# Optimization experiments

Hardware: AMD Instinct MI355X
Metric: run time of the kernel (lower is better)

## Reference

```python
import jax, jax.numpy as jnp
from jax import lax
import numpy as np

B = 32768      # batch
D = 256        # input = hidden = output dim
DEPTH = 9      # universal_depth


def setup_inputs() -> dict:
    key = jax.random.key(0)
    ks = jax.random.split(key, 16)
    s = 1.0 / np.sqrt(D)  # keep pre-activations sane
    r = lambda k, shp, sc=s: (jax.random.normal(k, shp, jnp.float32) * sc)
    return {
        "x": jax.random.normal(ks[0], (B, D), jnp.float32),
        "lin0_w": r(ks[1], (D, D)), "lin0_b": r(ks[2], (D,), 0.1),
        "lin1_w": r(ks[3], (D, D)), "lin1_b": r(ks[4], (D,), 0.1),
        "u1_w": jax.random.normal(ks[5], (DEPTH, D, D), jnp.float32),
        "u1_cw": r(ks[6], (D, D)), "u1_cb": r(ks[7], (D,), 0.1),
        "lin2_w": r(ks[8], (D, D)), "lin2_b": r(ks[9], (D,), 0.1),
        "u2_w": jax.random.normal(ks[10], (DEPTH, D, D), jnp.float32),
        "u2_cw": r(ks[11], (D, D)), "u2_cb": r(ks[12], (D,), 0.1),
        "lino_w": r(ks[13], (D, D)), "lino_b": r(ks[14], (D,), 0.1),
    }


def _universal_layer(x, uw, cw, cb):
    """UniversalNeuralLayer.forward, vectorized.

    The circulant 'gate' matrix implements, for state s of length n:
        s'[i] = cos*s[i] - sin*s[(i+1)%n] + sin*s[(i-1)%n]
    Applied 3 times per depth with angles uw[d, j, 0..2] (j = output unit).
    The result is independent of x and of the batch index.
    """
    n = x.shape[1]
    classical = x @ cw + cb                      # [B, n]
    # angle sequence per output j, in (depth, gate) order -> [3*DEPTH, n]
    angles = jnp.transpose(uw[:, :, :3], (0, 2, 1)).reshape(-1, n)
    init = jnp.full((n, n), 1.0 / np.sqrt(n), dtype=x.dtype)  # [n_j, n_state]

    def step(s, ang):
        c = jnp.cos(ang)[:, None]
        sn = jnp.sin(ang)[:, None]
        return c * s + sn * (jnp.roll(s, 1, axis=1) - jnp.roll(s, -1, axis=1)), None

    s, _ = lax.scan(step, init, angles)
    p = s[:, 0] ** 2                             # |state[0]|^2 per output j
    return jnp.tanh(classical + p[None, :])


def reference(x, lin0_w, lin0_b, lin1_w, lin1_b, u1_w, u1_cw, u1_cb,
              lin2_w, lin2_b, u2_w, u2_cw, u2_cb, lino_w, lino_b):
    h = jax.nn.relu(x @ lin0_w.T + lin0_b)
    h = jax.nn.relu(h @ lin1_w.T + lin1_b)
    h = _universal_layer(h, u1_w, u1_cw, u1_cb)
    h = jax.nn.relu(h @ lin2_w.T + lin2_b)
    h = _universal_layer(h, u2_w, u2_cw, u2_cb)
    return jax.nn.relu(h @ lino_w.T + lino_b)
```

## Files before the change

kernel.cpp:

```cpp
#include <hip/hip_runtime.h>
#include <math.h>

#define DD 256

typedef float  f32x4  __attribute__((ext_vector_type(4)));
typedef short  bf16x8 __attribute__((ext_vector_type(8)));

__device__ __forceinline__ unsigned short f2bf(float f) {
    unsigned int u = __float_as_uint(f);
    u = (u + 0x7fffu + ((u >> 16) & 1u)) >> 16;
    return (unsigned short)u;
}
__device__ __forceinline__ float bf2f(unsigned int h16) {
    return __uint_as_float(h16 << 16);
}

__global__ __launch_bounds__(256)
void universal_p_kernel(const float* __restrict__ u1_w,
                        const float* __restrict__ u2_w,
                        float* __restrict__ p_out ) {
    const int j = threadIdx.x;
    const float* uw = blockIdx.x ? u2_w : u1_w;
    float s = 0.0625f;
#pragma unroll
    for (int d = 0; d < 9; ++d)
#pragma unroll
        for (int g = 0; g < 3; ++g)
            s *= cosf(uw[d * DD * DD + j * DD + g]);
    p_out[blockIdx.x * DD + j] = s * s;
}

__global__ __launch_bounds__(256)
void prep_weights(const float* __restrict__ w0, const float* __restrict__ w1,
                  const float* __restrict__ cw1, const float* __restrict__ w2,
                  const float* __restrict__ cw2, const float* __restrict__ wo,
                  unsigned short* __restrict__ wall) {
    const int mat = blockIdx.y;
    const int n = blockIdx.x;
    const int k = threadIdx.x;
    const float* src;
    bool tr = false;
    switch (mat) {
        case 0: src = w0; break;
        case 1: src = w1; break;
        case 2: src = cw1; tr = true; break;
        case 3: src = w2; break;
        case 4: src = cw2; tr = true; break;
        default: src = wo; break;
    }
    const float v = tr ? src[k * DD + n] : src[n * DD + k];
    wall[mat * 65536 + n * DD + k] = f2bf(v);
}

__device__ __forceinline__ int chunk_idx(int m, int kc) {
    return kc * 64 + (m ^ (kc & 7));
}

__device__ __forceinline__ float fast_tanh(float x) {
    const float e = __expf(2.0f * x);
    return 1.0f - 2.0f * __builtin_amdgcn_rcpf(1.0f + e);
}

template <int MODE>
__device__ __forceinline__ void layer_step(const uint4* hc, uint4* hn,
                                           const unsigned short* __restrict__ W,
                                           const float* __restrict__ bias,
                                           const float* __restrict__ pv) {
    const int tid  = threadIdx.x;
    const int wave = tid >> 6;
    const int lane = tid & 63;
    const int quad = lane >> 4;
    const int l15  = lane & 15;
    const int nb   = wave * 64;

    f32x4 acc[4][4];
#pragma unroll
    for (int nt = 0; nt < 4; ++nt)
#pragma unroll
        for (int mt = 0; mt < 4; ++mt) acc[nt][mt] = (f32x4){0.f, 0.f, 0.f, 0.f};

    bf16x8 w_f[2][4], h_f[2][4];
    {
        const int koff = quad * 8;
#pragma unroll
        for (int nt = 0; nt < 4; ++nt)
            w_f[0][nt] = *(const bf16x8*)&W[(nb + nt * 16 + l15) * DD + koff];
#pragma unroll
        for (int mt = 0; mt < 4; ++mt)
            h_f[0][mt] = *(const bf16x8*)&hc[chunk_idx(mt * 16 + l15, quad)];
    }
#pragma unroll
    for (int k0 = 0; k0 < 8; ++k0) {
        const int cur = k0 & 1, nxt = cur ^ 1;
        if (k0 < 7) {
            const int kc = (k0 + 1) * 4 + quad;
#pragma unroll
            for (int nt = 0; nt < 4; ++nt)
                w_f[nxt][nt] = *(const bf16x8*)&W[(nb + nt * 16 + l15) * DD + kc * 8];
#pragma unroll
            for (int mt = 0; mt < 4; ++mt)
                h_f[nxt][mt] = *(const bf16x8*)&hc[chunk_idx(mt * 16 + l15, kc)];
        }
#pragma unroll
        for (int nt = 0; nt < 4; ++nt)
#pragma unroll
            for (int mt = 0; mt < 4; ++mt)
                acc[nt][mt] = __builtin_amdgcn_mfma_f32_16x16x32_bf16(
                    w_f[cur][nt], h_f[cur][mt], acc[nt][mt], 0, 0, 0);
    }

#pragma unroll
    for (int nt = 0; nt < 4; ++nt) {
        const int n0 = nb + nt * 16 + quad * 4;
        f32x4 add = *(const f32x4*)&bias[n0];
        if (MODE == 1) add += *(const f32x4*)&pv[n0];
        const int kc_o = n0 >> 3;
        const int half = quad & 1;
#pragma unroll
        for (int mt = 0; mt < 4; ++mt) {
            const f32x4 v = acc[nt][mt] + add;
            float t0, t1, t2, t3;
            if (MODE == 1) {
                t0 = fast_tanh(v.x); t1 = fast_tanh(v.y);
                t2 = fast_tanh(v.z); t3 = fast_tanh(v.w);
            } else {
                t0 = fmaxf(v.x, 0.f); t1 = fmaxf(v.y, 0.f);
                t2 = fmaxf(v.z, 0.f); t3 = fmaxf(v.w, 0.f);
            }
            uint2 u;
            u.x = (unsigned int)f2bf(t0) | ((unsigned int)f2bf(t1) << 16);
            u.y = (unsigned int)f2bf(t2) | ((unsigned int)f2bf(t3) << 16);
            *(uint2*)((char*)&hn[chunk_idx(mt * 16 + l15, kc_o)] + half * 8) = u;
        }
    }
    __syncthreads();
}

__global__ __launch_bounds__(256, 2)
void unet_fused(const float* __restrict__ x,
                const unsigned short* __restrict__ wall,
                const float* __restrict__ b0, const float* __restrict__ b1,
                const float* __restrict__ cb1, const float* __restrict__ b2,
                const float* __restrict__ cb2, const float* __restrict__ bo,
                const float* __restrict__ pbuf,
                float* __restrict__ out) {
    __shared__ uint4 h[2][2048];
    const int m0 = blockIdx.x * 64;
    const int tid = threadIdx.x;
    const int c4 = tid & 63;
    const int rbase = (tid >> 6) * 16;
    const int kc_s = c4 >> 1;
    const int half_s = c4 & 1;

#pragma unroll
    for (int i = 0; i < 16; ++i) {
        const int row = rbase + i;
        const float4 v = *(const float4*)&x[(size_t)(m0 + row) * DD + c4 * 4];
        uint2 u;
        u.x = (unsigned int)f2bf(v.x) | ((unsigned int)f2bf(v.y) << 16);
        u.y = (unsigned int)f2bf(v.z) | ((unsigned int)f2bf(v.w) << 16);
        *(uint2*)((char*)&h[0][chunk_idx(row, kc_s)] + half_s * 8) = u;
    }
    __syncthreads();

    layer_step<0>(h[0], h[1], wall + 0 * 65536, b0, nullptr);
    layer_step<0>(h[1], h[0], wall + 1 * 65536, b1, nullptr);
    layer_step<1>(h[0], h[1], wall + 2 * 65536, cb1, pbuf);
    layer_step<0>(h[1], h[0], wall + 3 * 65536, b2, nullptr);
    layer_step<1>(h[0], h[1], wall + 4 * 65536, cb2, pbuf + 256);
    layer_step<0>(h[1], h[0], wall + 5 * 65536, bo, nullptr);

#pragma unroll
    for (int i = 0; i < 16; ++i) {
        const int row = rbase + i;
        const uint2 u = *(const uint2*)((char*)&h[0][chunk_idx(row, kc_s)] + half_s * 8);
        float4 v;
        v.x = bf2f(u.x & 0xffffu); v.y = bf2f(u.x >> 16);
        v.z = bf2f(u.y & 0xffffu); v.w = bf2f(u.y >> 16);
        *(float4*)&out[(size_t)(m0 + row) * DD + c4 * 4] = v;
    }
}

extern "C" void kernel_launch(void* const* d_in, const int* in_sizes, int n_in,
                              void* d_out, int out_size, void* d_ws, size_t ws_size,
                              hipStream_t stream) {
    const float* x      = (const float*)d_in[0];
    const float* lin0_w = (const float*)d_in[1];
    const float* lin0_b = (const float*)d_in[2];
    const float* lin1_w = (const float*)d_in[3];
    const float* lin1_b = (const float*)d_in[4];
    const float* u1_w   = (const float*)d_in[5];
    const float* u1_cw  = (const float*)d_in[6];
    const float* u1_cb  = (const float*)d_in[7];
    const float* lin2_w = (const float*)d_in[8];
    const float* lin2_b = (const float*)d_in[9];
    const float* u2_w   = (const float*)d_in[10];
    const float* u2_cw  = (const float*)d_in[11];
    const float* u2_cb  = (const float*)d_in[12];
    const float* lino_w = (const float*)d_in[13];
    const float* lino_b = (const float*)d_in[14];

    float* out = (float*)d_out;
    unsigned short* wall = (unsigned short*)d_ws;
    float* pbuf = (float*)((char*)d_ws + 6 * 65536 * 2);

    universal_p_kernel<<<dim3(2), dim3(256), 0, stream>>>(u1_w, u2_w, pbuf);
    prep_weights<<<dim3(256, 6), dim3(256), 0, stream>>>(
        lin0_w, lin1_w, u1_cw, lin2_w, u2_cw, lino_w, wall);
    unet_fused<<<dim3(512), dim3(256), 0, stream>>>(
        x, wall, lin0_b, lin1_b, u1_cb, lin2_b, u2_cb, lino_b, pbuf, out);
}
```

Baseline: 178.0 us.

## Single LDS activation buffer with 3-stage weight register prefetch across layers

```diff
diff --git a/kernel.cpp b/kernel.cpp
--- a/kernel.cpp
+++ b/kernel.cpp
@@ -61,9 +61,19 @@
     return 1.0f - 2.0f * __builtin_amdgcn_rcpf(1.0f + e);
 }
 
-template <int MODE>
-__device__ __forceinline__ void layer_step(const uint4* hc, uint4* hn,
+__device__ __forceinline__ void prefetch_W(bf16x8 (&slot)[4],
                                            const unsigned short* __restrict__ W,
+                                           int k0, int nb, int l15, int quad) {
+    const int koff = k0 * 32 + quad * 8;
+#pragma unroll
+    for (int nt = 0; nt < 4; ++nt)
+        slot[nt] = *(const bf16x8*)&W[(nb + nt * 16 + l15) * DD + koff];
+}
+
+template <int PHASE, int MODE>
+__device__ __forceinline__ void layer_step(uint4* h, bf16x8 (&wr)[3][4],
+                                           const unsigned short* __restrict__ W,
+                                           const unsigned short* __restrict__ Wn,
                                            const float* __restrict__ bias,
                                            const float* __restrict__ pv) {
     const int tid  = threadIdx.x;
@@ -79,35 +89,33 @@
 #pragma unroll
         for (int mt = 0; mt < 4; ++mt) acc[nt][mt] = (f32x4){0.f, 0.f, 0.f, 0.f};
 
-    bf16x8 w_f[2][4], h_f[2][4];
-    {
-        const int koff = quad * 8;
-#pragma unroll
-        for (int nt = 0; nt < 4; ++nt)
-            w_f[0][nt] = *(const bf16x8*)&W[(nb + nt * 16 + l15) * DD + koff];
-#pragma unroll
-        for (int mt = 0; mt < 4; ++mt)
-            h_f[0][mt] = *(const bf16x8*)&hc[chunk_idx(mt * 16 + l15, quad)];
-    }
+    bf16x8 h_f[2][4];
+#pragma unroll
+    for (int mt = 0; mt < 4; ++mt)
+        h_f[0][mt] = *(const bf16x8*)&h[chunk_idx(mt * 16 + l15, quad)];
+
 #pragma unroll
     for (int k0 = 0; k0 < 8; ++k0) {
-        const int cur = k0 & 1, nxt = cur ^ 1;
+        const int cur = (PHASE + k0) % 3;
+        const int pf  = (PHASE + k0 + 2) % 3;
+        if (k0 < 6) prefetch_W(wr[pf], W, k0 + 2, nb, l15, quad);
+        else        prefetch_W(wr[pf], Wn, k0 - 6, nb, l15, quad);
         if (k0 < 7) {
             const int kc = (k0 + 1) * 4 + quad;
 #pragma unroll
-            for (int nt = 0; nt < 4; ++nt)
-                w_f[nxt][nt] = *(const bf16x8*)&W[(nb + nt * 16 + l15) * DD + kc * 8];
-#pragma unroll
             for (int mt = 0; mt < 4; ++mt)
-                h_f[nxt][mt] = *(const bf16x8*)&hc[chunk_idx(mt * 16 + l15, kc)];
+                h_f[(k0 + 1) & 1][mt] =
+                    *(const bf16x8*)&h[chunk_idx(mt * 16 + l15, kc)];
         }
 #pragma unroll
         for (int nt = 0; nt < 4; ++nt)
 #pragma unroll
             for (int mt = 0; mt < 4; ++mt)
                 acc[nt][mt] = __builtin_amdgcn_mfma_f32_16x16x32_bf16(
-                    w_f[cur][nt], h_f[cur][mt], acc[nt][mt], 0, 0, 0);
-    }
+                    wr[cur][nt], h_f[k0 & 1][mt], acc[nt][mt], 0, 0, 0);
+    }
+
+    __syncthreads();
 
 #pragma unroll
     for (int nt = 0; nt < 4; ++nt) {
@@ -130,13 +138,13 @@
             uint2 u;
             u.x = (unsigned int)f2bf(t0) | ((unsigned int)f2bf(t1) << 16);
             u.y = (unsigned int)f2bf(t2) | ((unsigned int)f2bf(t3) << 16);
-            *(uint2*)((char*)&hn[chunk_idx(mt * 16 + l15, kc_o)] + half * 8) = u;
+            *(uint2*)((char*)&h[chunk_idx(mt * 16 + l15, kc_o)] + half * 8) = u;
         }
     }
     __syncthreads();
 }
 
-__global__ __launch_bounds__(256, 2)
+__global__ __launch_bounds__(256, 3)
 void unet_fused(const float* __restrict__ x,
                 const unsigned short* __restrict__ wall,
                 const float* __restrict__ b0, const float* __restrict__ b1,
@@ -144,14 +152,23 @@
                 const float* __restrict__ cb2, const float* __restrict__ bo,
                 const float* __restrict__ pbuf,
                 float* __restrict__ out) {
-    __shared__ uint4 h[2][2048];
+    __shared__ uint4 h[2048];
     const int m0 = blockIdx.x * 64;
     const int tid = threadIdx.x;
+    const int wave = tid >> 6;
+    const int lane = tid & 63;
+    const int quad = lane >> 4;
+    const int l15  = lane & 15;
+    const int nb   = wave * 64;
+
+    bf16x8 wr[3][4];
+    prefetch_W(wr[0], wall, 0, nb, l15, quad);
+    prefetch_W(wr[1], wall, 1, nb, l15, quad);
+
     const int c4 = tid & 63;
     const int rbase = (tid >> 6) * 16;
     const int kc_s = c4 >> 1;
     const int half_s = c4 & 1;
-
 #pragma unroll
     for (int i = 0; i < 16; ++i) {
         const int row = rbase + i;
@@ -159,21 +176,21 @@
         uint2 u;
         u.x = (unsigned int)f2bf(v.x) | ((unsigned int)f2bf(v.y) << 16);
         u.y = (unsigned int)f2bf(v.z) | ((unsigned int)f2bf(v.w) << 16);
-        *(uint2*)((char*)&h[0][chunk_idx(row, kc_s)] + half_s * 8) = u;
+        *(uint2*)((char*)&h[chunk_idx(row, kc_s)] + half_s * 8) = u;
     }
     __syncthreads();
 
-    layer_step<0>(h[0], h[1], wall + 0 * 65536, b0, nullptr);
-    layer_step<0>(h[1], h[0], wall + 1 * 65536, b1, nullptr);
-    layer_step<1>(h[0], h[1], wall + 2 * 65536, cb1, pbuf);
-    layer_step<0>(h[1], h[0], wall + 3 * 65536, b2, nullptr);
-    layer_step<1>(h[0], h[1], wall + 4 * 65536, cb2, pbuf + 256);
-    layer_step<0>(h[1], h[0], wall + 5 * 65536, bo, nullptr);
+    layer_step<0, 0>(h, wr, wall + 0 * 65536, wall + 1 * 65536, b0, nullptr);
+    layer_step<2, 0>(h, wr, wall + 1 * 65536, wall + 2 * 65536, b1, nullptr);
+    layer_step<1, 1>(h, wr, wall + 2 * 65536, wall + 3 * 65536, cb1, pbuf);
+    layer_step<0, 0>(h, wr, wall + 3 * 65536, wall + 4 * 65536, b2, nullptr);
+    layer_step<2, 1>(h, wr, wall + 4 * 65536, wall + 5 * 65536, cb2, pbuf + 256);
+    layer_step<1, 0>(h, wr, wall + 5 * 65536, wall + 0 * 65536, bo, nullptr);
 
 #pragma unroll
     for (int i = 0; i < 16; ++i) {
         const int row = rbase + i;
-        const uint2 u = *(const uint2*)((char*)&h[0][chunk_idx(row, kc_s)] + half_s * 8);
+        const uint2 u = *(const uint2*)((char*)&h[chunk_idx(row, kc_s)] + half_s * 8);
         float4 v;
         v.x = bf2f(u.x & 0xffffu); v.y = bf2f(u.x >> 16);
         v.z = bf2f(u.y & 0xffffu); v.w = bf2f(u.y >> 16);
```

Result: slower. 195.1 us (+9.6%).

## Pre-swizzle weights into MFMA fragment order and shrink row tile to 32

Applied to the files above, without the earlier changes.

```diff
diff --git a/kernel.cpp b/kernel.cpp
--- a/kernel.cpp
+++ b/kernel.cpp
@@ -35,9 +35,18 @@
                   const float* __restrict__ cw1, const float* __restrict__ w2,
                   const float* __restrict__ cw2, const float* __restrict__ wo,
                   unsigned short* __restrict__ wall) {
-    const int mat = blockIdx.y;
-    const int n = blockIdx.x;
-    const int k = threadIdx.x;
+    const int gid  = blockIdx.x * 256 + threadIdx.x;
+    const int mat  = gid >> 13;
+    const int rem  = gid & 8191;
+    const int wb   = rem >> 11;
+    const int rem2 = rem & 2047;
+    const int k0   = rem2 >> 8;
+    const int rem3 = rem2 & 255;
+    const int nt   = rem3 >> 6;
+    const int lane = rem3 & 63;
+    const int n  = wb * 64 + nt * 16 + (lane & 15);
+    const int kb = k0 * 32 + (lane >> 4) * 8;
+
     const float* src;
     bool tr = false;
     switch (mat) {
@@ -48,12 +57,18 @@
         case 4: src = cw2; tr = true; break;
         default: src = wo; break;
     }
-    const float v = tr ? src[k * DD + n] : src[n * DD + k];
-    wall[mat * 65536 + n * DD + k] = f2bf(v);
+    unsigned short tmp[8];
+#pragma unroll
+    for (int j = 0; j < 8; ++j) {
+        const float v = tr ? src[(kb + j) * DD + n] : src[n * DD + kb + j];
+        tmp[j] = f2bf(v);
+    }
+    *(uint4*)&wall[mat * 65536 + wb * 16384 + k0 * 2048 + nt * 512 + lane * 8] =
+        *(const uint4*)tmp;
 }
 
 __device__ __forceinline__ int chunk_idx(int m, int kc) {
-    return kc * 64 + (m ^ (kc & 7));
+    return kc * 32 + (m ^ (kc & 7));
 }
 
 __device__ __forceinline__ float fast_tanh(float x) {
@@ -62,8 +77,9 @@
 }
 
 template <int MODE>
-__device__ __forceinline__ void layer_step(const uint4* hc, uint4* hn,
+__device__ __forceinline__ void layer_step(uint4* h, bf16x8 (&wr)[2][4],
                                            const unsigned short* __restrict__ W,
+                                           const unsigned short* __restrict__ Wn,
                                            const float* __restrict__ bias,
                                            const float* __restrict__ pv) {
     const int tid  = threadIdx.x;
@@ -71,44 +87,46 @@
     const int lane = tid & 63;
     const int quad = lane >> 4;
     const int l15  = lane & 15;
-    const int nb   = wave * 64;
-
-    f32x4 acc[4][4];
+    const unsigned short* Wb  = W  + wave * 16384 + lane * 8;
+    const unsigned short* Wnb = Wn + wave * 16384 + lane * 8;
+
+    f32x4 acc[4][2];
 #pragma unroll
     for (int nt = 0; nt < 4; ++nt)
 #pragma unroll
-        for (int mt = 0; mt < 4; ++mt) acc[nt][mt] = (f32x4){0.f, 0.f, 0.f, 0.f};
-
-    bf16x8 w_f[2][4], h_f[2][4];
-    {
-        const int koff = quad * 8;
-#pragma unroll
-        for (int nt = 0; nt < 4; ++nt)
-            w_f[0][nt] = *(const bf16x8*)&W[(nb + nt * 16 + l15) * DD + koff];
-#pragma unroll
-        for (int mt = 0; mt < 4; ++mt)
-            h_f[0][mt] = *(const bf16x8*)&hc[chunk_idx(mt * 16 + l15, quad)];
-    }
+        for (int mt = 0; mt < 2; ++mt) acc[nt][mt] = (f32x4){0.f, 0.f, 0.f, 0.f};
+
+    bf16x8 h_f[2][2];
+#pragma unroll
+    for (int mt = 0; mt < 2; ++mt)
+        h_f[0][mt] = *(const bf16x8*)&h[chunk_idx(mt * 16 + l15, quad)];
+
 #pragma unroll
     for (int k0 = 0; k0 < 8; ++k0) {
         const int cur = k0 & 1, nxt = cur ^ 1;
+        {
+            const unsigned short* ws = (k0 < 7) ? &Wb[(k0 + 1) * 2048] : Wnb;
+#pragma unroll
+            for (int nt = 0; nt < 4; ++nt)
+                wr[nxt][nt] = *(const bf16x8*)&ws[nt * 512];
+        }
         if (k0 < 7) {
             const int kc = (k0 + 1) * 4 + quad;
 #pragma unroll
-            for (int nt = 0; nt < 4; ++nt)
-                w_f[nxt][nt] = *(const bf16x8*)&W[(nb + nt * 16 + l15) * DD + kc * 8];
-#pragma unroll
-            for (int mt = 0; mt < 4; ++mt)
-                h_f[nxt][mt] = *(const bf16x8*)&hc[chunk_idx(mt * 16 + l15, kc)];
+            for (int mt = 0; mt < 2; ++mt)
+                h_f[nxt][mt] = *(const bf16x8*)&h[chunk_idx(mt * 16 + l15, kc)];
         }
 #pragma unroll
         for (int nt = 0; nt < 4; ++nt)
 #pragma unroll
-            for (int mt = 0; mt < 4; ++mt)
+            for (int mt = 0; mt < 2; ++mt)
                 acc[nt][mt] = __builtin_amdgcn_mfma_f32_16x16x32_bf16(
-                    w_f[cur][nt], h_f[cur][mt], acc[nt][mt], 0, 0, 0);
-    }
-
+                    wr[cur][nt], h_f[cur][mt], acc[nt][mt], 0, 0, 0);
+    }
+
+    __syncthreads();
+
+    const int nb = wave * 64;
 #pragma unroll
     for (int nt = 0; nt < 4; ++nt) {
         const int n0 = nb + nt * 16 + quad * 4;
@@ -117,7 +135,7 @@
         const int kc_o = n0 >> 3;
         const int half = quad & 1;
 #pragma unroll
-        for (int mt = 0; mt < 4; ++mt) {
+        for (int mt = 0; mt < 2; ++mt) {
             const f32x4 v = acc[nt][mt] + add;
             float t0, t1, t2, t3;
             if (MODE == 1) {
@@ -130,7 +148,7 @@
             uint2 u;
             u.x = (unsigned int)f2bf(t0) | ((unsigned int)f2bf(t1) << 16);
             u.y = (unsigned int)f2bf(t2) | ((unsigned int)f2bf(t3) << 16);
-            *(uint2*)((char*)&hn[chunk_idx(mt * 16 + l15, kc_o)] + half * 8) = u;
+            *(uint2*)((char*)&h[chunk_idx(mt * 16 + l15, kc_o)] + half * 8) = u;
         }
     }
     __syncthreads();
@@ -144,36 +162,46 @@
                 const float* __restrict__ cb2, const float* __restrict__ bo,
                 const float* __restrict__ pbuf,
                 float* __restrict__ out) {
-    __shared__ uint4 h[2][2048];
-    const int m0 = blockIdx.x * 64;
+    __shared__ uint4 h[1024];
+    const int m0 = blockIdx.x * 32;
     const int tid = threadIdx.x;
+    const int wave = tid >> 6;
+    const int lane = tid & 63;
+
+    bf16x8 wr[2][4];
+    {
+        const unsigned short* ws = wall + wave * 16384 + lane * 8;
+#pragma unroll
+        for (int nt = 0; nt < 4; ++nt)
+            wr[0][nt] = *(const bf16x8*)&ws[nt * 512];
+    }
+
     const int c4 = tid & 63;
-    const int rbase = (tid >> 6) * 16;
+    const int rbase = (tid >> 6) * 8;
     const int kc_s = c4 >> 1;
     const int half_s = c4 & 1;
-
-#pragma unroll
-    for (int i = 0; i < 16; ++i) {
+#pragma unroll
+    for (int i = 0; i < 8; ++i) {
         const int row = rbase + i;
         const float4 v = *(const float4*)&x[(size_t)(m0 + row) * DD + c4 * 4];
         uint2 u;
         u.x = (unsigned int)f2bf(v.x) | ((unsigned int)f2bf(v.y) << 16);
         u.y = (unsigned int)f2bf(v.z) | ((unsigned int)f2bf(v.w) << 16);
-        *(uint2*)((char*)&h[0][chunk_idx(row, kc_s)] + half_s * 8) = u;
+        *(uint2*)((char*)&h[chunk_idx(row, kc_s)] + half_s * 8) = u;
     }
     __syncthreads();
 
-    layer_step<0>(h[0], h[1], wall + 0 * 65536, b0, nullptr);
-    layer_step<0>(h[1], h[0], wall + 1 * 65536, b1, nullptr);
-    layer_step<1>(h[0], h[1], wall + 2 * 65536, cb1, pbuf);
-    layer_step<0>(h[1], h[0], wall + 3 * 65536, b2, nullptr);
-    layer_step<1>(h[0], h[1], wall + 4 * 65536, cb2, pbuf + 256);
-    layer_step<0>(h[1], h[0], wall + 5 * 65536, bo, nullptr);
-
-#pragma unroll
-    for (int i = 0; i < 16; ++i) {
+    layer_step<0>(h, wr, wall + 0 * 65536, wall + 1 * 65536, b0, nullptr);
+    layer_step<0>(h, wr, wall + 1 * 65536, wall + 2 * 65536, b1, nullptr);
+    layer_step<1>(h, wr, wall + 2 * 65536, wall + 3 * 65536, cb1, pbuf);
+    layer_step<0>(h, wr, wall + 3 * 65536, wall + 4 * 65536, b2, nullptr);
+    layer_step<1>(h, wr, wall + 4 * 65536, wall + 5 * 65536, cb2, pbuf + 256);
+    layer_step<0>(h, wr, wall + 5 * 65536, wall + 0 * 65536, bo, nullptr);
+
+#pragma unroll
+    for (int i = 0; i < 8; ++i) {
         const int row = rbase + i;
-        const uint2 u = *(const uint2*)((char*)&h[0][chunk_idx(row, kc_s)] + half_s * 8);
+        const uint2 u = *(const uint2*)((char*)&h[chunk_idx(row, kc_s)] + half_s * 8);
         float4 v;
         v.x = bf2f(u.x & 0xffffu); v.y = bf2f(u.x >> 16);
         v.z = bf2f(u.y & 0xffffu); v.w = bf2f(u.y >> 16);
@@ -205,8 +233,8 @@
     float* pbuf = (float*)((char*)d_ws + 6 * 65536 * 2);
 
     universal_p_kernel<<<dim3(2), dim3(256), 0, stream>>>(u1_w, u2_w, pbuf);
-    prep_weights<<<dim3(256, 6), dim3(256), 0, stream>>>(
+    prep_weights<<<dim3(192), dim3(256), 0, stream>>>(
         lin0_w, lin1_w, u1_cw, lin2_w, u2_cw, lino_w, wall);
-    unet_fused<<<dim3(512), dim3(256), 0, stream>>>(
+    unet_fused<<<dim3(1024), dim3(256), 0, stream>>>(
         x, wall, lin0_b, lin1_b, u1_cb, lin2_b, u2_cb, lino_b, pbuf, out);
 }
```

Result: faster. 153.1 us (-14.0%).
